# Performance work log

Measured on AMD Instinct MI355X. Metric: run time of the kernel, lower is better.

The kernel has to match this reference:

```python
import jax, jax.numpy as jnp
import numpy as np

D_MODEL = 1024
N_HEADS = 16
D_K = 64
D_V = 64
LN_EPS = 1e-5


def setup_inputs() -> dict:
    key = jax.random.key(0)
    ks = jax.random.split(key, 12)
    B, S = 2, 2048
    s_in = 1.0 / np.sqrt(D_MODEL)
    s_out = 1.0 / np.sqrt(N_HEADS * D_V)
    Q = jax.random.normal(ks[0], (B, S, D_MODEL), dtype=jnp.float32)
    K = jax.random.normal(ks[1], (B, S, D_MODEL), dtype=jnp.float32)
    V = jax.random.normal(ks[2], (B, S, D_MODEL), dtype=jnp.float32)
    attn_mask = jnp.zeros((B, S, S), dtype=bool)
    Wq = jax.random.normal(ks[3], (D_MODEL, N_HEADS * D_K), dtype=jnp.float32) * s_in
    bq = jnp.zeros((N_HEADS * D_K,), dtype=jnp.float32)
    Wk = jax.random.normal(ks[4], (D_MODEL, N_HEADS * D_K), dtype=jnp.float32) * s_in
    bk = jnp.zeros((N_HEADS * D_K,), dtype=jnp.float32)
    Wv = jax.random.normal(ks[5], (D_MODEL, N_HEADS * D_V), dtype=jnp.float32) * s_in
    bv = jnp.zeros((N_HEADS * D_V,), dtype=jnp.float32)
    Wo = jax.random.normal(ks[6], (N_HEADS * D_V, D_MODEL), dtype=jnp.float32) * s_out
    bo = jnp.zeros((D_MODEL,), dtype=jnp.float32)
    gamma = jnp.ones((D_MODEL,), dtype=jnp.float32)
    beta = jnp.zeros((D_MODEL,), dtype=jnp.float32)
    return {"Q": Q, "K": K, "V": V, "attn_mask": attn_mask,
            "Wq": Wq, "bq": bq, "Wk": Wk, "bk": bk, "Wv": Wv, "bv": bv,
            "Wo": Wo, "bo": bo, "gamma": gamma, "beta": beta}


def _layer_norm(x, gamma, beta):
    mu = jnp.mean(x, axis=-1, keepdims=True)
    var = jnp.mean(jnp.square(x - mu), axis=-1, keepdims=True)
    return (x - mu) * jax.lax.rsqrt(var + LN_EPS) * gamma + beta


def reference(Q, K, V, attn_mask, Wq, bq, Wk, bk, Wv, bv, Wo, bo, gamma, beta):
    B, S, _ = Q.shape
    # projections -> [B, H, S, d]
    Qs = (Q @ Wq + bq).reshape(B, S, N_HEADS, D_K).transpose(0, 2, 1, 3)
    Ks = (K @ Wk + bk).reshape(B, S, N_HEADS, D_K).transpose(0, 2, 1, 3)
    Vs = (V @ Wv + bv).reshape(B, S, N_HEADS, D_V).transpose(0, 2, 1, 3)
    # scores [B, H, Sq, Sk]
    scores = jnp.einsum("bhqd,bhkd->bhqk", Qs, Ks) / np.sqrt(D_K).astype(np.float32)
    scores = jnp.where(attn_mask[:, None, :, :], jnp.float32(-1e9), scores)
    attn = jax.nn.softmax(scores, axis=-1)
    context = jnp.einsum("bhqk,bhkd->bhqd", attn, Vs)
    context = context.transpose(0, 2, 1, 3).reshape(B, S, N_HEADS * D_V)
    output = context @ Wo + bo
    output = _layer_norm(output + Q, gamma, beta)
    return (output, attn)
```

## Files before the change

### kernel.cpp

```cpp
#include <hip/hip_runtime.h>
#include <hip/hip_bf16.h>

#define S_LEN 2048
#define NH 16
#define HD 64
#define DM 1024

typedef float f32x4 __attribute__((ext_vector_type(4)));
typedef unsigned u32x4 __attribute__((ext_vector_type(4)));
typedef unsigned u32x2 __attribute__((ext_vector_type(2)));
typedef __bf16 bf16x8 __attribute__((ext_vector_type(8)));

#define BAR() __builtin_amdgcn_s_barrier()
#define VMCNT(N) asm volatile("s_waitcnt vmcnt(" #N ")" ::: "memory")

__device__ __forceinline__ unsigned short f2bf(float f) {
  union { float f; unsigned u; } v; v.f = f;
  unsigned r = v.u + 0x7fffu + ((v.u >> 16) & 1u);
  return (unsigned short)(r >> 16);
}

__device__ __forceinline__ unsigned pack2bf(float lo, float hi) {
  return (unsigned)f2bf(lo) | ((unsigned)f2bf(hi) << 16);
}

__device__ __forceinline__ void load_lds16(const void* g, void* l) {
  __builtin_amdgcn_global_load_lds((const __attribute__((address_space(1))) void*)g,
                                   (__attribute__((address_space(3))) void*)l, 16, 0, 0);
}

__global__ __launch_bounds__(256) void prep_kernel(const float* __restrict__ Qi,
                                                   const float* __restrict__ Ki,
                                                   const float* __restrict__ Vi,
                                                   unsigned short* __restrict__ Qb,
                                                   unsigned short* __restrict__ Kb,
                                                   unsigned short* __restrict__ Vb,
                                                   const float* __restrict__ Wq,
                                                   const float* __restrict__ Wk,
                                                   const float* __restrict__ Wv,
                                                   const float* __restrict__ Wo,
                                                   unsigned short* __restrict__ Wtq,
                                                   unsigned short* __restrict__ Wtk,
                                                   unsigned short* __restrict__ Wtv,
                                                   unsigned short* __restrict__ Wto) {
  __shared__ float t[32][33];
  const int bid = blockIdx.x;
  if (bid < 12288) {
    int sel = bid >> 12;
    int i = (bid & 4095) * 256 + threadIdx.x;
    const float* in = sel == 0 ? Qi : (sel == 1 ? Ki : Vi);
    unsigned short* out = sel == 0 ? Qb : (sel == 1 ? Kb : Vb);
    float4 v = reinterpret_cast<const float4*>(in)[i];
    ushort4 o;
    o.x = f2bf(v.x); o.y = f2bf(v.y); o.z = f2bf(v.z); o.w = f2bf(v.w);
    reinterpret_cast<ushort4*>(out)[i] = o;
  } else {
    int r = bid - 12288;
    int wi = r >> 10, ti = r & 1023;
    const float* W = wi == 0 ? Wq : (wi == 1 ? Wk : (wi == 2 ? Wv : Wo));
    unsigned short* Wt = wi == 0 ? Wtq : (wi == 1 ? Wtk : (wi == 2 ? Wtv : Wto));
    int bx = (ti & 31) * 32;
    int by = (ti >> 5) * 32;
    int tx = threadIdx.x & 31, ty = threadIdx.x >> 5;
    for (int i = ty; i < 32; i += 8) t[i][tx] = W[(size_t)(by + i) * DM + bx + tx];
    __syncthreads();
    for (int i = ty; i < 32; i += 8) Wt[(size_t)(bx + i) * DM + by + tx] = f2bf(t[tx][i]);
  }
}

__global__ __launch_bounds__(256) void gemm_qkv(const unsigned short* __restrict__ Qb,
                                                const unsigned short* __restrict__ Kb,
                                                const unsigned short* __restrict__ Vb,
                                                const unsigned short* __restrict__ Wtq,
                                                const unsigned short* __restrict__ Wtk,
                                                const unsigned short* __restrict__ Wtv,
                                                const float* __restrict__ bq,
                                                const float* __restrict__ bk,
                                                const float* __restrict__ bv,
                                                unsigned short* __restrict__ Qhd,
                                                unsigned short* __restrict__ Khd,
                                                unsigned short* __restrict__ Vtd) {
  constexpr int K = 1024;
  __shared__ unsigned short Al[128 * 32];
  __shared__ unsigned short Bl[128 * 32];
  const int z = blockIdx.z;
  const unsigned short* A = z == 0 ? Qb : (z == 1 ? Kb : Vb);
  const unsigned short* Bt = z == 0 ? Wtq : (z == 1 ? Wtk : Wtv);
  const float* bias = z == 0 ? bq : (z == 1 ? bk : bv);
  unsigned short* C = z == 0 ? Qhd : (z == 1 ? Khd : Vtd);
  const int tid = threadIdx.x;
  const int w = tid >> 6, l = tid & 63;
  const int m0 = blockIdx.x * 128, n0 = blockIdx.y * 128;
  const int wr = (w >> 1) * 64, wc = (w & 1) * 64;
  const int lr = l & 15, lk = l >> 4;
  f32x4 acc[4][4] = {};
  for (int kt = 0; kt < K; kt += 32) {
#pragma unroll
    for (int i = 0; i < 2; ++i) {
      int seg = i * 256 + tid;
      int row = seg >> 2, ks = (seg & 3) * 8;
      load_lds16(A + (size_t)(m0 + row) * K + kt + ks, Al + seg * 8);
      load_lds16(Bt + (size_t)(n0 + row) * K + kt + ks, Bl + seg * 8);
    }
    __syncthreads();
    bf16x8 af[4], bfr[4];
#pragma unroll
    for (int t = 0; t < 4; ++t) af[t] = *(const bf16x8*)(Al + (wr + t * 16 + lr) * 32 + lk * 8);
#pragma unroll
    for (int t = 0; t < 4; ++t) bfr[t] = *(const bf16x8*)(Bl + (wc + t * 16 + lr) * 32 + lk * 8);
#pragma unroll
    for (int i = 0; i < 4; ++i)
#pragma unroll
      for (int j = 0; j < 4; ++j)
        acc[i][j] = __builtin_amdgcn_mfma_f32_16x16x32_bf16(af[i], bfr[j], acc[i][j], 0, 0, 0);
    __syncthreads();
  }
  const int drow = lk * 4, dcol = lr;
  if (z < 2) {
#pragma unroll
    for (int i = 0; i < 4; ++i)
#pragma unroll
      for (int j = 0; j < 4; ++j) {
        int n = n0 + wc + j * 16 + dcol;
        float bv_ = bias[n];
        int h = n >> 6, d = n & 63;
#pragma unroll
        for (int r = 0; r < 4; ++r) {
          int m = m0 + wr + i * 16 + drow + r;
          int b = m >> 11, s = m & 2047;
          C[((size_t)(b * NH + h) * S_LEN + s) * HD + d] = f2bf(acc[i][j][r] + bv_);
        }
      }
  } else {
#pragma unroll
    for (int i = 0; i < 4; ++i) {
      int m = m0 + wr + i * 16 + drow;
      int b = m >> 11, s = m & 2047;
#pragma unroll
      for (int j = 0; j < 4; ++j) {
        int n = n0 + wc + j * 16 + dcol;
        float bv_ = bias[n];
        int h = n >> 6, d = n & 63;
        ushort4 o;
        o.x = f2bf(acc[i][j][0] + bv_);
        o.y = f2bf(acc[i][j][1] + bv_);
        o.z = f2bf(acc[i][j][2] + bv_);
        o.w = f2bf(acc[i][j][3] + bv_);
        *reinterpret_cast<ushort4*>(C + ((size_t)(b * NH + h) * HD + d) * S_LEN + s) = o;
      }
    }
  }
}

__global__ __launch_bounds__(256) void gemm_out(const unsigned short* __restrict__ A,
                                                const unsigned short* __restrict__ Bt,
                                                const float* __restrict__ bias,
                                                float* __restrict__ C) {
  constexpr int K = 1024;
  constexpr int N = 1024;
  __shared__ unsigned short Al[128 * 32];
  __shared__ unsigned short Bl[64 * 32];
  const int tid = threadIdx.x;
  const int w = tid >> 6, l = tid & 63;
  const int m0 = blockIdx.x * 128, n0 = blockIdx.y * 64;
  const int wr = (w >> 1) * 64, wc = (w & 1) * 32;
  const int lr = l & 15, lk = l >> 4;
  f32x4 acc[4][2] = {};
  for (int kt = 0; kt < K; kt += 32) {
#pragma unroll
    for (int i = 0; i < 2; ++i) {
      int seg = i * 256 + tid;
      int row = seg >> 2, ks = (seg & 3) * 8;
      load_lds16(A + (size_t)(m0 + row) * K + kt + ks, Al + seg * 8);
    }
    {
      int row = tid >> 2, ks = (tid & 3) * 8;
      load_lds16(Bt + (size_t)(n0 + row) * K + kt + ks, Bl + tid * 8);
    }
    __syncthreads();
    bf16x8 af[4], bfr[2];
#pragma unroll
    for (int t = 0; t < 4; ++t) af[t] = *(const bf16x8*)(Al + (wr + t * 16 + lr) * 32 + lk * 8);
#pragma unroll
    for (int t = 0; t < 2; ++t) bfr[t] = *(const bf16x8*)(Bl + (wc + t * 16 + lr) * 32 + lk * 8);
#pragma unroll
    for (int i = 0; i < 4; ++i)
#pragma unroll
      for (int j = 0; j < 2; ++j)
        acc[i][j] = __builtin_amdgcn_mfma_f32_16x16x32_bf16(af[i], bfr[j], acc[i][j], 0, 0, 0);
    __syncthreads();
  }
  const int drow = lk * 4, dcol = lr;
#pragma unroll
  for (int i = 0; i < 4; ++i)
#pragma unroll
    for (int j = 0; j < 2; ++j) {
      int n = n0 + wc + j * 16 + dcol;
      float bv = bias[n];
#pragma unroll
      for (int r = 0; r < 4; ++r) {
        int m = m0 + wr + i * 16 + drow + r;
        C[(size_t)m * N + n] = acc[i][j][r] + bv;
      }
    }
}

#define STG_K(T, BASE)                                                         \
  {                                                                            \
    int s_ = tid;                                                              \
    int row_ = s_ >> 3, cb_ = (s_ & 7) * 16;                                   \
    load_lds16((const char*)Kbh + (size_t)((T) * 64 + row_) * 128 +            \
                   (cb_ ^ ((row_ & 7) << 4)),                                  \
               (BASE) + s_ * 16);                                              \
  }

#define STG_V(T, BASE)                                                         \
  {                                                                            \
    int s_ = tid;                                                              \
    int row_ = s_ >> 3, cb_ = (s_ & 7) * 16;                                   \
    load_lds16((const char*)Vbh + (size_t)row_ * 4096 + (T) * 128 +            \
                   (cb_ ^ ((row_ & 7) << 4)),                                  \
               (BASE) + s_ * 16);                                              \
  }

#define QKT4(KPTR)                                                             \
  _Pragma("unroll") for (int st = 0; st < 4; ++st) {                           \
    const char* rp = (KPTR) + (st * 16 + lr) * 128;                            \
    bf16x8 k0 = *(const bf16x8*)(rp + a0);                                     \
    bf16x8 k1 = *(const bf16x8*)(rp + (a0 ^ 64));                              \
    f32x4 a = {};                                                              \
    a = __builtin_amdgcn_mfma_f32_16x16x32_bf16(k0, qf0, a, 0, 0, 0);          \
    a = __builtin_amdgcn_mfma_f32_16x16x32_bf16(k1, qf1, a, 0, 0, 0);          \
    acc[st] = a;                                                               \
  }

#define MASKADJ4(T)                                                            \
  _Pragma("unroll") for (int st = 0; st < 4; ++st) {                           \
    uchar4 m4 = *(const uchar4*)(mrow + (T) * 64 + st * 16 + lk * 4);          \
    if (m4.x) acc[st][0] = -8e9f;                                              \
    if (m4.y) acc[st][1] = -8e9f;                                              \
    if (m4.z) acc[st][2] = -8e9f;                                              \
    if (m4.w) acc[st][3] = -8e9f;                                              \
  }

#define MASK_PREPASS()                                                         \
  unsigned maskbits = 0;                                                       \
  _Pragma("unroll") for (int g4 = 0; g4 < 4; ++g4) {                           \
    unsigned mm[8];                                                            \
    const char* mp = (const char*)mrow + g4 * 512 + lk * 16;                   \
    _Pragma("unroll") for (int q8 = 0; q8 < 8; ++q8) {                         \
      u32x4 v = __builtin_nontemporal_load((const u32x4*)(mp + q8 * 64));      \
      mm[q8] = v.x | v.y | v.z | v.w;                                          \
    }                                                                          \
    _Pragma("unroll") for (int q8 = 0; q8 < 8; ++q8)                           \
      if (__any(mm[q8] != 0)) maskbits |= 1u << (g4 * 8 + q8);                 \
  }

__global__ __launch_bounds__(512, 4) void attn_fused_kernel(const unsigned short* __restrict__ Qh,
                                                            const unsigned short* __restrict__ Kh,
                                                            const unsigned short* __restrict__ Vt,
                                                            const unsigned char* __restrict__ mask,
                                                            float* __restrict__ attn_out,
                                                            unsigned short* __restrict__ ctx) {
  __shared__ char lds[81920];
  char* const ldsK = lds;
  char* const ldsV = lds + 24576;
  const int tid = threadIdx.x;
  const int w = tid >> 6, l = tid & 63;
  const int lr = l & 15, lk = l >> 4;
  const int L = blockIdx.x;
  const int g = L & 7, j = L >> 3;
  const int bh = g * 4 + (j & 3);
  const int qt = j >> 2;
  const int q0w = qt * 128 + w * 16;
  const int b = bh >> 4, h = bh & 15;
  const unsigned short* Qbh = Qh + (size_t)bh * S_LEN * HD;
  const unsigned short* Kbh = Kh + (size_t)bh * S_LEN * HD;
  const unsigned short* Vbh = Vt + (size_t)bh * HD * S_LEN;
  const unsigned char* mrow = mask + (size_t)b * S_LEN * S_LEN + (size_t)(q0w + lr) * S_LEN;
  char* const abase = (char*)(attn_out + ((size_t)bh * S_LEN + q0w) * S_LEN);

  bf16x8 qf0 = *(const bf16x8*)(Qbh + (q0w + lr) * HD + lk * 8);
  bf16x8 qf1 = *(const bf16x8*)(Qbh + (q0w + lr) * HD + 32 + lk * 8);
  const int sw = (lr & 7) << 4;
  const int a0 = (lk * 16) ^ sw;
  const float sc = 0.125f;

  MASK_PREPASS()

  f32x4 acc[4];
  f32x4 cacc[4] = {};
  float tsum = 0.f;

  {
    int cur = 0, stg = 2;
    STG_K(0, ldsK)
    STG_V(0, ldsV)
    STG_K(1, ldsK + 8192)
    STG_V(1, ldsV + 8192)
    for (int t = 0; t < 32; ++t) {
      BAR();
      if (t < 30) {
        STG_K(t + 2, ldsK + stg * 8192)
        STG_V(t + 2, ldsV + stg * 8192)
      }
      if (t < 30) { VMCNT(4); }
      else if (t == 30) { VMCNT(2); }
      else { VMCNT(0); }
      BAR();
      const char* Kp = ldsK + cur * 8192;
      const char* Vp = ldsV + cur * 8192;
      QKT4(Kp)
      if (maskbits & (1u << t)) { MASKADJ4(t) }
      unsigned pk0[4], pk1[4];
#pragma unroll
      for (int st = 0; st < 4; ++st) {
        float p0 = __expf(acc[st][0] * sc);
        float p1 = __expf(acc[st][1] * sc);
        float p2 = __expf(acc[st][2] * sc);
        float p3 = __expf(acc[st][3] * sc);
        tsum += p0 + p1 + p2 + p3;
        pk0[st] = pack2bf(p0, p1);
        pk1[st] = pack2bf(p2, p3);
      }
      char* Pw = lds + 49152 + (w * 2 + (t & 1)) * 2048;
#pragma unroll
      for (int st = 0; st < 4; ++st) {
        u32x2 pv;
        pv.x = pk0[st];
        pv.y = pk1[st];
        *(u32x2*)(Pw + lr * 128 + ((st * 32 + lk * 8) ^ sw)) = pv;
      }
      asm volatile("s_waitcnt lgkmcnt(0)" ::: "memory");
      __builtin_amdgcn_sched_barrier(0);
#pragma unroll
      for (int c = 0; c < 2; ++c) {
        bf16x8 af = *(const bf16x8*)(Pw + lr * 128 + ((c * 64 + lk * 16) ^ sw));
        const int voff = (c * 64 + lk * 16) ^ sw;
#pragma unroll
        for (int dt = 0; dt < 4; ++dt) {
          bf16x8 vb = *(const bf16x8*)(Vp + (dt * 16 + lr) * 128 + voff);
          cacc[dt] = __builtin_amdgcn_mfma_f32_16x16x32_bf16(af, vb, cacc[dt], 0, 0, 0);
        }
      }
      cur = cur == 2 ? 0 : cur + 1;
      stg = stg == 2 ? 0 : stg + 1;
    }
  }
  tsum += __shfl_xor(tsum, 16, 64);
  tsum += __shfl_xor(tsum, 32, 64);
  const float linv = 1.0f / tsum;

#pragma unroll
  for (int dt = 0; dt < 4; ++dt)
#pragma unroll
    for (int r = 0; r < 4; ++r)
      ctx[(size_t)(b * S_LEN + q0w + lk * 4 + r) * DM + h * HD + dt * 16 + lr] =
          f2bf(cacc[dt][r] * linv);

  BAR();
  char* const Pw2 = lds + w * 8192;
  const int swp = lr << 4;
  for (int tt = 0; tt < 16; ++tt) {
#pragma unroll
    for (int half = 0; half < 2; ++half) {
      const int t = tt * 2 + half;
      bf16x8 kf0[4], kf1[4];
#pragma unroll
      for (int st = 0; st < 4; ++st) {
        const unsigned short* kp = Kbh + (size_t)(t * 64 + st * 16 + lr) * HD + lk * 8;
        kf0[st] = *(const bf16x8*)kp;
        kf1[st] = *(const bf16x8*)(kp + 32);
      }
#pragma unroll
      for (int st = 0; st < 4; ++st) {
        f32x4 a = {};
        a = __builtin_amdgcn_mfma_f32_16x16x32_bf16(kf0[st], qf0, a, 0, 0, 0);
        a = __builtin_amdgcn_mfma_f32_16x16x32_bf16(kf1[st], qf1, a, 0, 0, 0);
        acc[st] = a;
      }
      if (maskbits & (1u << t)) { MASKADJ4(t) }
#pragma unroll
      for (int st = 0; st < 4; ++st) {
        f32x4 p;
        p.x = __expf(acc[st][0] * sc) * linv;
        p.y = __expf(acc[st][1] * sc) * linv;
        p.z = __expf(acc[st][2] * sc) * linv;
        p.w = __expf(acc[st][3] * sc) * linv;
        *(f32x4*)(Pw2 + lr * 512 + ((half * 256 + st * 64 + lk * 16) ^ swp)) = p;
      }
    }
    asm volatile("s_waitcnt lgkmcnt(0)" ::: "memory");
    __builtin_amdgcn_sched_barrier(0);
#pragma unroll
    for (int s = 0; s < 8; ++s) {
      const int row = s * 2 + (l >> 5);
      const int ch = (l & 31) * 16;
      f32x4 v = *(const f32x4*)(Pw2 + row * 512 + (ch ^ (row << 4)));
      __builtin_nontemporal_store(v, (f32x4*)(abase + (size_t)row * 8192 + tt * 512 + ch));
    }
  }
}

__global__ __launch_bounds__(256) void ln_kernel(const float* __restrict__ pre,
                                                 const float* __restrict__ Qin,
                                                 const float* __restrict__ gamma,
                                                 const float* __restrict__ beta,
                                                 float* __restrict__ out) {
  __shared__ float red[4];
  const int row = blockIdx.x;
  const int tid = threadIdx.x;
  const int wv = tid >> 6, l = tid & 63;
  const float4 a = reinterpret_cast<const float4*>(pre + (size_t)row * DM)[tid];
  const float4 q = reinterpret_cast<const float4*>(Qin + (size_t)row * DM)[tid];
  float x0 = a.x + q.x, x1 = a.y + q.y, x2 = a.z + q.z, x3 = a.w + q.w;
  float s = x0 + x1 + x2 + x3;
#pragma unroll
  for (int off = 32; off >= 1; off >>= 1) s += __shfl_xor(s, off, 64);
  if (l == 0) red[wv] = s;
  __syncthreads();
  float mean = (red[0] + red[1] + red[2] + red[3]) * (1.0f / 1024.0f);
  __syncthreads();
  float d0 = x0 - mean, d1 = x1 - mean, d2 = x2 - mean, d3 = x3 - mean;
  float s2 = d0 * d0 + d1 * d1 + d2 * d2 + d3 * d3;
#pragma unroll
  for (int off = 32; off >= 1; off >>= 1) s2 += __shfl_xor(s2, off, 64);
  if (l == 0) red[wv] = s2;
  __syncthreads();
  float var = (red[0] + red[1] + red[2] + red[3]) * (1.0f / 1024.0f);
  float rstd = rsqrtf(var + 1e-5f);
  const float4 g = reinterpret_cast<const float4*>(gamma)[tid];
  const float4 bt = reinterpret_cast<const float4*>(beta)[tid];
  float4 o;
  o.x = d0 * rstd * g.x + bt.x;
  o.y = d1 * rstd * g.y + bt.y;
  o.z = d2 * rstd * g.z + bt.z;
  o.w = d3 * rstd * g.w + bt.w;
  reinterpret_cast<float4*>(out + (size_t)row * DM)[tid] = o;
}

extern "C" void kernel_launch(void* const* d_in, const int* in_sizes, int n_in,
                              void* d_out, int out_size, void* d_ws, size_t ws_size,
                              hipStream_t stream) {
  const float* Qi = (const float*)d_in[0];
  const float* Ki = (const float*)d_in[1];
  const float* Vi = (const float*)d_in[2];
  const unsigned char* mask = (const unsigned char*)d_in[3];
  const float* Wq = (const float*)d_in[4];
  const float* bq = (const float*)d_in[5];
  const float* Wk = (const float*)d_in[6];
  const float* bk = (const float*)d_in[7];
  const float* Wv = (const float*)d_in[8];
  const float* bv = (const float*)d_in[9];
  const float* Wo = (const float*)d_in[10];
  const float* bo = (const float*)d_in[11];
  const float* gamma = (const float*)d_in[12];
  const float* beta = (const float*)d_in[13];

  char* ws = (char*)d_ws;
  unsigned short* Qb = (unsigned short*)(ws);
  unsigned short* Kb = Qb + 4194304;
  unsigned short* Vb = Qb + 2 * 4194304;
  unsigned short* Wtq = (unsigned short*)(ws + 25165824);
  unsigned short* Wtk = Wtq + 1048576;
  unsigned short* Wtv = Wtq + 2 * 1048576;
  unsigned short* Wto = Wtq + 3 * 1048576;
  unsigned short* Qhd = (unsigned short*)(ws + 33554432);
  unsigned short* Khd = (unsigned short*)(ws + 41943040);
  unsigned short* Vtd = (unsigned short*)(ws + 50331648);
  unsigned short* ctx = (unsigned short*)(ws);
  float* preLN = (float*)(ws + 8388608);

  float* out0 = (float*)d_out;
  float* attn = out0 + 4194304;

  prep_kernel<<<16384, 256, 0, stream>>>(Qi, Ki, Vi, Qb, Kb, Vb,
                                         Wq, Wk, Wv, Wo, Wtq, Wtk, Wtv, Wto);
  dim3 gqkv(32, 8, 3);
  gemm_qkv<<<gqkv, 256, 0, stream>>>(Qb, Kb, Vb, Wtq, Wtk, Wtv,
                                     bq, bk, bv, Qhd, Khd, Vtd);
  attn_fused_kernel<<<512, 512, 0, stream>>>(Qhd, Khd, Vtd, mask, attn, ctx);
  dim3 gg(32, 16);
  gemm_out<<<gg, 256, 0, stream>>>(ctx, Wto, bo, preLN);
  ln_kernel<<<4096, 256, 0, stream>>>(preLN, Qi, gamma, beta, out0);
}
```

Baseline: 300.5 us.

## Drop LDS triple-buffered K/V staging; load K and V fragments directly from global

Removes the cooperative global-to-LDS triple-buffered pipeline for K and V tiles in the first attention pass, along with its block-wide barriers and vmcnt waits. Each wave now loads its K and V MFMA fragments straight from global memory (relying on L1/L2 reuse across the 8 waves), and the per-wave P scratch no longer double-buffers. LDS shrinks from 80KB to 64KB, which may allow more resident blocks. The cost is redundant global/cache traffic per wave and exposed load latency with no explicit prefetch. The V loads now read a strided transposed layout uncoalesced per lane.

```diff
diff --git a/kernel.cpp b/kernel.cpp
--- a/kernel.cpp
+++ b/kernel.cpp
@@ -12,7 +12,6 @@
 typedef __bf16 bf16x8 __attribute__((ext_vector_type(8)));
 
 #define BAR() __builtin_amdgcn_s_barrier()
-#define VMCNT(N) asm volatile("s_waitcnt vmcnt(" #N ")" ::: "memory")
 
 __device__ __forceinline__ unsigned short f2bf(float f) {
   union { float f; unsigned u; } v; v.f = f;
@@ -205,32 +204,18 @@
     }
 }
 
-#define STG_K(T, BASE)                                                         \
-  {                                                                            \
-    int s_ = tid;                                                              \
-    int row_ = s_ >> 3, cb_ = (s_ & 7) * 16;                                   \
-    load_lds16((const char*)Kbh + (size_t)((T) * 64 + row_) * 128 +            \
-                   (cb_ ^ ((row_ & 7) << 4)),                                  \
-               (BASE) + s_ * 16);                                              \
-  }
-
-#define STG_V(T, BASE)                                                         \
-  {                                                                            \
-    int s_ = tid;                                                              \
-    int row_ = s_ >> 3, cb_ = (s_ & 7) * 16;                                   \
-    load_lds16((const char*)Vbh + (size_t)row_ * 4096 + (T) * 128 +            \
-                   (cb_ ^ ((row_ & 7) << 4)),                                  \
-               (BASE) + s_ * 16);                                              \
-  }
-
-#define QKT4(KPTR)                                                             \
+#define LOADK_R(T)                                                             \
   _Pragma("unroll") for (int st = 0; st < 4; ++st) {                           \
-    const char* rp = (KPTR) + (st * 16 + lr) * 128;                            \
-    bf16x8 k0 = *(const bf16x8*)(rp + a0);                                     \
-    bf16x8 k1 = *(const bf16x8*)(rp + (a0 ^ 64));                              \
+    const unsigned short* kp = Kbh + (size_t)((T) * 64 + st * 16 + lr) * HD + lk * 8; \
+    kf0[st] = *(const bf16x8*)kp;                                              \
+    kf1[st] = *(const bf16x8*)(kp + 32);                                       \
+  }
+
+#define QKT_R()                                                                \
+  _Pragma("unroll") for (int st = 0; st < 4; ++st) {                           \
     f32x4 a = {};                                                              \
-    a = __builtin_amdgcn_mfma_f32_16x16x32_bf16(k0, qf0, a, 0, 0, 0);          \
-    a = __builtin_amdgcn_mfma_f32_16x16x32_bf16(k1, qf1, a, 0, 0, 0);          \
+    a = __builtin_amdgcn_mfma_f32_16x16x32_bf16(kf0[st], qf0, a, 0, 0, 0);     \
+    a = __builtin_amdgcn_mfma_f32_16x16x32_bf16(kf1[st], qf1, a, 0, 0, 0);     \
     acc[st] = a;                                                               \
   }
 
@@ -262,9 +247,7 @@
                                                             const unsigned char* __restrict__ mask,
                                                             float* __restrict__ attn_out,
                                                             unsigned short* __restrict__ ctx) {
-  __shared__ char lds[81920];
-  char* const ldsK = lds;
-  char* const ldsV = lds + 24576;
+  __shared__ char lds[65536];
   const int tid = threadIdx.x;
   const int w = tid >> 6, l = tid & 63;
   const int lr = l & 15, lk = l >> 4;
@@ -283,68 +266,49 @@
   bf16x8 qf0 = *(const bf16x8*)(Qbh + (q0w + lr) * HD + lk * 8);
   bf16x8 qf1 = *(const bf16x8*)(Qbh + (q0w + lr) * HD + 32 + lk * 8);
   const int sw = (lr & 7) << 4;
-  const int a0 = (lk * 16) ^ sw;
   const float sc = 0.125f;
 
   MASK_PREPASS()
 
   f32x4 acc[4];
+  bf16x8 kf0[4], kf1[4];
   f32x4 cacc[4] = {};
   float tsum = 0.f;
 
-  {
-    int cur = 0, stg = 2;
-    STG_K(0, ldsK)
-    STG_V(0, ldsV)
-    STG_K(1, ldsK + 8192)
-    STG_V(1, ldsV + 8192)
-    for (int t = 0; t < 32; ++t) {
-      BAR();
-      if (t < 30) {
-        STG_K(t + 2, ldsK + stg * 8192)
-        STG_V(t + 2, ldsV + stg * 8192)
+  char* const Pw = lds + w * 2048;
+  for (int t = 0; t < 32; ++t) {
+    LOADK_R(t)
+    QKT_R()
+    if (maskbits & (1u << t)) { MASKADJ4(t) }
+    unsigned pk0[4], pk1[4];
+#pragma unroll
+    for (int st = 0; st < 4; ++st) {
+      float p0 = __expf(acc[st][0] * sc);
+      float p1 = __expf(acc[st][1] * sc);
+      float p2 = __expf(acc[st][2] * sc);
+      float p3 = __expf(acc[st][3] * sc);
+      tsum += p0 + p1 + p2 + p3;
+      pk0[st] = pack2bf(p0, p1);
+      pk1[st] = pack2bf(p2, p3);
+    }
+#pragma unroll
+    for (int st = 0; st < 4; ++st) {
+      u32x2 pv;
+      pv.x = pk0[st];
+      pv.y = pk1[st];
+      *(u32x2*)(Pw + lr * 128 + ((st * 32 + lk * 8) ^ sw)) = pv;
+    }
+    asm volatile("s_waitcnt lgkmcnt(0)" ::: "memory");
+    __builtin_amdgcn_sched_barrier(0);
+#pragma unroll
+    for (int c = 0; c < 2; ++c) {
+      bf16x8 af = *(const bf16x8*)(Pw + lr * 128 + ((c * 64 + lk * 16) ^ sw));
+#pragma unroll
+      for (int dt = 0; dt < 4; ++dt) {
+        bf16x8 vb = *(const bf16x8*)(Vbh + (size_t)(dt * 16 + lr) * S_LEN +
+                                     t * 64 + c * 32 + lk * 8);
+        cacc[dt] = __builtin_amdgcn_mfma_f32_16x16x32_bf16(af, vb, cacc[dt], 0, 0, 0);
       }
-      if (t < 30) { VMCNT(4); }
-      else if (t == 30) { VMCNT(2); }
-      else { VMCNT(0); }
-      BAR();
-      const char* Kp = ldsK + cur * 8192;
-      const char* Vp = ldsV + cur * 8192;
-      QKT4(Kp)
-      if (maskbits & (1u << t)) { MASKADJ4(t) }
-      unsigned pk0[4], pk1[4];
-#pragma unroll
-      for (int st = 0; st < 4; ++st) {
-        float p0 = __expf(acc[st][0] * sc);
-        float p1 = __expf(acc[st][1] * sc);
-        float p2 = __expf(acc[st][2] * sc);
-        float p3 = __expf(acc[st][3] * sc);
-        tsum += p0 + p1 + p2 + p3;
-        pk0[st] = pack2bf(p0, p1);
-        pk1[st] = pack2bf(p2, p3);
-      }
-      char* Pw = lds + 49152 + (w * 2 + (t & 1)) * 2048;
-#pragma unroll
-      for (int st = 0; st < 4; ++st) {
-        u32x2 pv;
-        pv.x = pk0[st];
-        pv.y = pk1[st];
-        *(u32x2*)(Pw + lr * 128 + ((st * 32 + lk * 8) ^ sw)) = pv;
-      }
-      asm volatile("s_waitcnt lgkmcnt(0)" ::: "memory");
-      __builtin_amdgcn_sched_barrier(0);
-#pragma unroll
-      for (int c = 0; c < 2; ++c) {
-        bf16x8 af = *(const bf16x8*)(Pw + lr * 128 + ((c * 64 + lk * 16) ^ sw));
-        const int voff = (c * 64 + lk * 16) ^ sw;
-#pragma unroll
-        for (int dt = 0; dt < 4; ++dt) {
-          bf16x8 vb = *(const bf16x8*)(Vp + (dt * 16 + lr) * 128 + voff);
-          cacc[dt] = __builtin_amdgcn_mfma_f32_16x16x32_bf16(af, vb, cacc[dt], 0, 0, 0);
-        }
-      }
-      cur = cur == 2 ? 0 : cur + 1;
-      stg = stg == 2 ? 0 : stg + 1;
     }
   }
   tsum += __shfl_xor(tsum, 16, 64);
@@ -365,20 +329,8 @@
 #pragma unroll
     for (int half = 0; half < 2; ++half) {
       const int t = tt * 2 + half;
-      bf16x8 kf0[4], kf1[4];
-#pragma unroll
-      for (int st = 0; st < 4; ++st) {
-        const unsigned short* kp = Kbh + (size_t)(t * 64 + st * 16 + lr) * HD + lk * 8;
-        kf0[st] = *(const bf16x8*)kp;
-        kf1[st] = *(const bf16x8*)(kp + 32);
-      }
-#pragma unroll
-      for (int st = 0; st < 4; ++st) {
-        f32x4 a = {};
-        a = __builtin_amdgcn_mfma_f32_16x16x32_bf16(kf0[st], qf0, a, 0, 0, 0);
-        a = __builtin_amdgcn_mfma_f32_16x16x32_bf16(kf1[st], qf1, a, 0, 0, 0);
-        acc[st] = a;
-      }
+      LOADK_R(t)
+      QKT_R()
       if (maskbits & (1u << t)) { MASKADJ4(t) }
 #pragma unroll
       for (int st = 0; st < 4; ++st) {
```

New measurement: 486.8 us. 1.62x slower.

## Stage 128-key K/V tiles with double buffering instead of 64-key triple buffering

Applied to the files above, without the earlier changes.

The attention loop now stages 128 keys of K and V per iteration into two LDS buffers and processes each staged tile as two 64-key halves. This halves the number of barrier pairs and wait points per block while keeping one tile of prefetch ahead. The trade-off is a shallower prefetch (one tile ahead instead of two) and a single P scratch buffer per wave, which may expose load latency more.

```diff
diff --git a/kernel.cpp b/kernel.cpp
--- a/kernel.cpp
+++ b/kernel.cpp
@@ -205,25 +205,25 @@
     }
 }
 
-#define STG_K(T, BASE)                                                         \
-  {                                                                            \
-    int s_ = tid;                                                              \
+#define STG_K128(T, BASE)                                                      \
+  _Pragma("unroll") for (int i_ = 0; i_ < 2; ++i_) {                           \
+    int s_ = i_ * 512 + tid;                                                   \
     int row_ = s_ >> 3, cb_ = (s_ & 7) * 16;                                   \
-    load_lds16((const char*)Kbh + (size_t)((T) * 64 + row_) * 128 +            \
+    load_lds16((const char*)Kbh + (size_t)((T) * 128 + row_) * 128 +           \
                    (cb_ ^ ((row_ & 7) << 4)),                                  \
                (BASE) + s_ * 16);                                              \
   }
 
-#define STG_V(T, BASE)                                                         \
-  {                                                                            \
-    int s_ = tid;                                                              \
-    int row_ = s_ >> 3, cb_ = (s_ & 7) * 16;                                   \
-    load_lds16((const char*)Vbh + (size_t)row_ * 4096 + (T) * 128 +            \
+#define STG_V128(T, BASE)                                                      \
+  _Pragma("unroll") for (int i_ = 0; i_ < 2; ++i_) {                           \
+    int s_ = i_ * 512 + tid;                                                   \
+    int row_ = s_ >> 4, cb_ = (s_ & 15) * 16;                                  \
+    load_lds16((const char*)Vbh + (size_t)row_ * 4096 + (T) * 256 +            \
                    (cb_ ^ ((row_ & 7) << 4)),                                  \
                (BASE) + s_ * 16);                                              \
   }
 
-#define QKT4(KPTR)                                                             \
+#define QKT4H(KPTR)                                                            \
   _Pragma("unroll") for (int st = 0; st < 4; ++st) {                           \
     const char* rp = (KPTR) + (st * 16 + lr) * 128;                            \
     bf16x8 k0 = *(const bf16x8*)(rp + a0);                                     \
@@ -264,7 +264,7 @@
                                                             unsigned short* __restrict__ ctx) {
   __shared__ char lds[81920];
   char* const ldsK = lds;
-  char* const ldsV = lds + 24576;
+  char* const ldsV = lds + 32768;
   const int tid = threadIdx.x;
   const int w = tid >> 6, l = tid & 63;
   const int lr = l & 15, lk = l >> 4;
@@ -293,58 +293,56 @@
   float tsum = 0.f;
 
   {
-    int cur = 0, stg = 2;
-    STG_K(0, ldsK)
-    STG_V(0, ldsV)
-    STG_K(1, ldsK + 8192)
-    STG_V(1, ldsV + 8192)
-    for (int t = 0; t < 32; ++t) {
+    STG_K128(0, ldsK)
+    STG_V128(0, ldsV)
+    char* const Pw = lds + 65536 + w * 2048;
+    for (int T = 0; T < 16; ++T) {
+      const int buf = T & 1;
       BAR();
-      if (t < 30) {
-        STG_K(t + 2, ldsK + stg * 8192)
-        STG_V(t + 2, ldsV + stg * 8192)
-      }
-      if (t < 30) { VMCNT(4); }
-      else if (t == 30) { VMCNT(2); }
-      else { VMCNT(0); }
+      if (T < 15) {
+        STG_K128(T + 1, ldsK + (buf ^ 1) * 16384)
+        STG_V128(T + 1, ldsV + (buf ^ 1) * 16384)
+      }
+      if (T < 15) { VMCNT(4); } else { VMCNT(0); }
       BAR();
-      const char* Kp = ldsK + cur * 8192;
-      const char* Vp = ldsV + cur * 8192;
-      QKT4(Kp)
-      if (maskbits & (1u << t)) { MASKADJ4(t) }
-      unsigned pk0[4], pk1[4];
-#pragma unroll
-      for (int st = 0; st < 4; ++st) {
-        float p0 = __expf(acc[st][0] * sc);
-        float p1 = __expf(acc[st][1] * sc);
-        float p2 = __expf(acc[st][2] * sc);
-        float p3 = __expf(acc[st][3] * sc);
-        tsum += p0 + p1 + p2 + p3;
-        pk0[st] = pack2bf(p0, p1);
-        pk1[st] = pack2bf(p2, p3);
-      }
-      char* Pw = lds + 49152 + (w * 2 + (t & 1)) * 2048;
-#pragma unroll
-      for (int st = 0; st < 4; ++st) {
-        u32x2 pv;
-        pv.x = pk0[st];
-        pv.y = pk1[st];
-        *(u32x2*)(Pw + lr * 128 + ((st * 32 + lk * 8) ^ sw)) = pv;
-      }
-      asm volatile("s_waitcnt lgkmcnt(0)" ::: "memory");
-      __builtin_amdgcn_sched_barrier(0);
-#pragma unroll
-      for (int c = 0; c < 2; ++c) {
-        bf16x8 af = *(const bf16x8*)(Pw + lr * 128 + ((c * 64 + lk * 16) ^ sw));
-        const int voff = (c * 64 + lk * 16) ^ sw;
-#pragma unroll
-        for (int dt = 0; dt < 4; ++dt) {
-          bf16x8 vb = *(const bf16x8*)(Vp + (dt * 16 + lr) * 128 + voff);
-          cacc[dt] = __builtin_amdgcn_mfma_f32_16x16x32_bf16(af, vb, cacc[dt], 0, 0, 0);
+#pragma unroll
+      for (int half = 0; half < 2; ++half) {
+        const int t = 2 * T + half;
+        const char* Kp = ldsK + buf * 16384 + half * 8192;
+        const char* Vp = ldsV + buf * 16384;
+        QKT4H(Kp)
+        if (maskbits & (1u << t)) { MASKADJ4(t) }
+        unsigned pk0[4], pk1[4];
+#pragma unroll
+        for (int st = 0; st < 4; ++st) {
+          float p0 = __expf(acc[st][0] * sc);
+          float p1 = __expf(acc[st][1] * sc);
+          float p2 = __expf(acc[st][2] * sc);
+          float p3 = __expf(acc[st][3] * sc);
+          tsum += p0 + p1 + p2 + p3;
+          pk0[st] = pack2bf(p0, p1);
+          pk1[st] = pack2bf(p2, p3);
         }
-      }
-      cur = cur == 2 ? 0 : cur + 1;
-      stg = stg == 2 ? 0 : stg + 1;
+#pragma unroll
+        for (int st = 0; st < 4; ++st) {
+          u32x2 pv;
+          pv.x = pk0[st];
+          pv.y = pk1[st];
+          *(u32x2*)(Pw + lr * 128 + ((st * 32 + lk * 8) ^ sw)) = pv;
+        }
+        asm volatile("s_waitcnt lgkmcnt(0)" ::: "memory");
+        __builtin_amdgcn_sched_barrier(0);
+#pragma unroll
+        for (int c = 0; c < 2; ++c) {
+          bf16x8 af = *(const bf16x8*)(Pw + lr * 128 + ((c * 64 + lk * 16) ^ sw));
+          const int voff = (half * 128 + c * 64 + lk * 16) ^ sw;
+#pragma unroll
+          for (int dt = 0; dt < 4; ++dt) {
+            bf16x8 vb = *(const bf16x8*)(Vp + (dt * 16 + lr) * 256 + voff);
+            cacc[dt] = __builtin_amdgcn_mfma_f32_16x16x32_bf16(af, vb, cacc[dt], 0, 0, 0);
+          }
+        }
+      }
     }
   }
   tsum += __shfl_xor(tsum, 16, 64);
```

Result: no change. 298.6 us (-0.6%).
